# Optimization experiments

Measured on AMD Instinct MI355X. Metric: run time of the kernel, lower is better.

The kernel has to match this reference:

```python
import jax, jax.numpy as jnp
import numpy as np

B, S, DIN, DOUT, A, T, H = 8, 1024, 1024, 1024, 4, 4, 8  # arity A, T cell types, hidden H


def setup_inputs() -> dict:
    key = jax.random.key(0)
    ks = jax.random.split(key, 6)
    x = jax.random.normal(ks[0], (B, S, DIN), jnp.float32)
    sc = 1.0 / np.sqrt(DIN).astype(np.float32)
    weight = jax.random.uniform(ks[1], (A * DOUT, DIN), jnp.float32, -sc, sc)
    bias = jax.random.uniform(ks[2], (A * DOUT,), jnp.float32, -sc, sc)
    # stacked per-cell-type MLP params: arity -> H -> 1 (tanh)
    cw1 = jax.random.normal(ks[3], (T, A, H), jnp.float32) / np.sqrt(A).astype(np.float32)
    cb1 = jnp.zeros((T, H), jnp.float32)
    cw2 = jax.random.normal(ks[4], (T, H), jnp.float32) / np.sqrt(H).astype(np.float32)
    cb2 = jnp.zeros((T,), jnp.float32)
    return {"x": x, "weight": weight, "bias": bias,
            "cw1": cw1, "cb1": cb1, "cw2": cw2, "cb2": cb2}


def reference(x, weight, bias, cw1, cb1, cw2, cb2):
    T_, A_, H_ = cw1.shape
    Dout = weight.shape[0] // A_
    G = Dout // T_  # neurons per cell type (cell_indices = contiguous blocks via np.repeat)
    # all_inputs = F.linear(input, weight, bias): (B, S, A*Dout)
    z = jnp.einsum('bsd,od->bso', x, weight) + bias
    # slice per-neuron arity chunks -> (B, S, T, G, A)
    z = z.reshape(z.shape[0], z.shape[1], T_, G, A_)
    # per-cell-type MLP applied to every neuron of that type (replaces Python loop)
    h = jnp.tanh(jnp.einsum('bstga,tah->bstgh', z, cw1) + cb1[:, None, :])
    o = jnp.einsum('bstgh,th->bstg', h, cw2) + cb2[:, None]
    # concat over neurons -> (B, S, Dout)
    return o.reshape(o.shape[0], o.shape[1], Dout)
```

## Files before the change

kernel.cpp:

```cpp
#include <hip/hip_runtime.h>


typedef __bf16 bf16x8 __attribute__((ext_vector_type(8)));
typedef float f32x4 __attribute__((ext_vector_type(4)));
typedef float f32x16 __attribute__((ext_vector_type(16)));

#define BM 256
#define BN 128
#define BK 32
#define KDIM 1024
#define NT 32
#define ABUF 16384
#define BUFB 24576
#define XN8 (8192 * 1024 / 8)
#define WN8 (4096 * 1024 / 8)

__global__ __launch_bounds__(256) void cvt_bf16_kernel(
    const float* __restrict__ x, const float* __restrict__ w,
    __bf16* __restrict__ xb, __bf16* __restrict__ wb) {
    int i = blockIdx.x * 256 + threadIdx.x;
    const float* src;
    __bf16* dst;
    int j, jdst;
    if (i < XN8) { src = x; dst = xb; j = i; jdst = i; }
    else {
        src = w; dst = wb; j = i - XN8;
        const int r  = j >> 7;
        const int c8 = j & 127;
        const int q  = r >> 2;
        const int a  = r & 3;
        const int rn = ((q >> 5) << 7) + (a << 5) + (q & 31);
        jdst = (rn << 7) + c8;
    }
    const f32x4* p = (const f32x4*)src + 2 * (size_t)j;
    f32x4 a = p[0], b = p[1];
    bf16x8 o;
    o[0] = (__bf16)a[0]; o[1] = (__bf16)a[1]; o[2] = (__bf16)a[2]; o[3] = (__bf16)a[3];
    o[4] = (__bf16)b[0]; o[5] = (__bf16)b[1]; o[6] = (__bf16)b[2]; o[7] = (__bf16)b[3];
    ((bf16x8*)dst)[jdst] = o;
}

__global__ __launch_bounds__(256, 2) void fused_gemm_mlp_kernel(
    const __bf16* __restrict__ Ag,
    const __bf16* __restrict__ Bg,
    const float* __restrict__ bias,
    const float* __restrict__ cw1,
    const float* __restrict__ cb1,
    const float* __restrict__ cw2,
    const float* __restrict__ cb2,
    float* __restrict__ out)
{
    __shared__ __align__(16) unsigned char raw[2 * BUFB];

    const int tid  = threadIdx.x;
    const int wave = tid >> 6;
    const int lane = tid & 63;
    const int wm = wave;
    const int bn0 = blockIdx.x * BN;
    const int bm0 = blockIdx.y * BM;

    f32x16 acc[2][4] = {};

    const int qloc = lane >> 3;
    const int slog = (lane & 7) ^ qloc;
    const int arow = 2 * qloc + (slog >> 2);
    const int acol = (slog & 3) * 8;

    const int lr5 = lane & 31;
    const int lk2 = lane >> 5;
    const int lrh = lr5 >> 1;
    const int lp  = lr5 & 1;
    int a_addr[2], b_addr[2];
#pragma unroll
    for (int kh = 0; kh < 2; ++kh) {
        const int slot = (((lp * 4) + (kh * 2 + lk2)) ^ (lrh & 7)) * 16;
        a_addr[kh] = wm * 4096 + lrh * 128 + slot;
        b_addr[kh] = ABUF + lrh * 128 + slot;
    }
    const char* sb = (const char*)raw;

    auto stage = [&](int t) {
        const int bb = (t & 1) * BUFB;
        const int k0 = t * BK;
#pragma unroll
        for (int c = 0; c < 4; ++c) {
            const int ch = wave + c * 4;
            const __bf16* g = Ag + (size_t)(bm0 + ch * 16 + arow) * KDIM + k0 + acol;
            __builtin_amdgcn_global_load_lds(
                (__attribute__((address_space(1))) void*)g,
                (__attribute__((address_space(3))) void*)&raw[bb + ch * 1024],
                16, 0, 0);
        }
#pragma unroll
        for (int c = 0; c < 2; ++c) {
            const int ch = wave + c * 4;
            const __bf16* g = Bg + (size_t)(bn0 + ch * 16 + arow) * KDIM + k0 + acol;
            __builtin_amdgcn_global_load_lds(
                (__attribute__((address_space(1))) void*)g,
                (__attribute__((address_space(3))) void*)&raw[bb + ABUF + ch * 1024],
                16, 0, 0);
        }
    };

    stage(0);
    __syncthreads();

    for (int t = 0; t < NT; ++t) {
        if (t + 1 < NT) stage(t + 1);

        const int cb = (t & 1) * BUFB;
#pragma unroll
        for (int kh = 0; kh < 2; ++kh) {
            bf16x8 af[2], bfr[4];
#pragma unroll
            for (int mi = 0; mi < 2; ++mi)
                af[mi] = *(const bf16x8*)(sb + cb + a_addr[kh] + mi * 2048);
#pragma unroll
            for (int a = 0; a < 4; ++a)
                bfr[a] = *(const bf16x8*)(sb + cb + b_addr[kh] + a * 2048);
#pragma unroll
            for (int mi = 0; mi < 2; ++mi)
#pragma unroll
                for (int a = 0; a < 4; ++a)
                    acc[mi][a] = __builtin_amdgcn_mfma_f32_32x32x16_bf16(
                        af[mi], bfr[a], acc[mi][a], 0, 0, 0);
        }
        __syncthreads();
    }

    const int tct = bn0 >> 10;
    float w1[32], b1[8], w2[8];
#pragma unroll
    for (int i = 0; i < 32; ++i) w1[i] = cw1[tct * 32 + i];
#pragma unroll
    for (int i = 0; i < 8; ++i) { b1[i] = cb1[tct * 8 + i]; w2[i] = cw2[tct * 8 + i]; }
    const float b2 = cb2[tct];

    const f32x4 bz = *(const f32x4*)&bias[bn0 + 4 * lr5];

    const float L2E2 = 2.885390081777927f;
    float* outp = out + (size_t)(bm0 + wm * 64 + 4 * lk2) * 1024 + (bn0 >> 2) + lr5;

#pragma unroll
    for (int mi = 0; mi < 2; ++mi) {
#pragma unroll
        for (int g = 0; g < 16; ++g) {
            const float z0 = acc[mi][0][g] + bz[0];
            const float z1 = acc[mi][1][g] + bz[1];
            const float z2 = acc[mi][2][g] + bz[2];
            const float z3 = acc[mi][3][g] + bz[3];
            float o = 0.f;
#pragma unroll
            for (int hh = 0; hh < 8; ++hh) {
                float pre = z0 * w1[0 * 8 + hh] + z1 * w1[1 * 8 + hh]
                          + z2 * w1[2 * 8 + hh] + z3 * w1[3 * 8 + hh] + b1[hh];
                float e = __builtin_amdgcn_exp2f(pre * L2E2);
                float th = 1.0f - 2.0f * __builtin_amdgcn_rcpf(e + 1.0f);
                o += th * w2[hh];
            }
            o += b2;
            const int row = mi * 32 + (g & 3) + 8 * (g >> 2);
            outp[(size_t)row * 1024] = o;
        }
    }
}

extern "C" void kernel_launch(void* const* d_in, const int* in_sizes, int n_in,
                              void* d_out, int out_size, void* d_ws, size_t ws_size,
                              hipStream_t stream) {
    const float* x    = (const float*)d_in[0];
    const float* w    = (const float*)d_in[1];
    const float* bias = (const float*)d_in[2];
    const float* cw1  = (const float*)d_in[3];
    const float* cb1  = (const float*)d_in[4];
    const float* cw2  = (const float*)d_in[5];
    const float* cb2  = (const float*)d_in[6];
    float* out = (float*)d_out;

    __bf16* xb = (__bf16*)d_ws;
    __bf16* wb = xb + (size_t)8192 * 1024;

    cvt_bf16_kernel<<<(XN8 + WN8) / 256, 256, 0, stream>>>(x, w, xb, wb);

    dim3 grid(4096 / BN, 8192 / BM);
    fused_gemm_mlp_kernel<<<grid, 256, 0, stream>>>(xb, wb, bias, cw1, cb1, cw2, cb2, out);
}
```

Before: 190.5 us.

## Load weight fragments directly from global in MFMA order, double BK

The convert kernel now writes the bf16 weight in a layout already ordered as MFMA B-fragments, so the GEMM kernel reads B operands straight from global memory (through L1/L2) instead of staging them in LDS. The K tile doubles to 64, halving the iteration count and barrier count, and LDS holds only the A tile. This removes B's LDS traffic and staging work, but each wave now issues global loads on the critical MFMA path, which may expose latency because there is no explicit prefetch.

```diff
diff --git a/kernel.cpp b/kernel.cpp
--- a/kernel.cpp
+++ b/kernel.cpp
@@ -7,11 +7,10 @@
 
 #define BM 256
 #define BN 128
-#define BK 32
+#define BK 64
 #define KDIM 1024
-#define NT 32
-#define ABUF 16384
-#define BUFB 24576
+#define NT 16
+#define ABUF 32768
 #define XN8 (8192 * 1024 / 8)
 #define WN8 (4096 * 1024 / 8)
 
@@ -29,8 +28,12 @@
         const int c8 = j & 127;
         const int q  = r >> 2;
         const int a  = r & 3;
-        const int rn = ((q >> 5) << 7) + (a << 5) + (q & 31);
-        jdst = (rn << 7) + c8;
+        const int nb = q >> 5;
+        const int l5 = q & 31;
+        const int kt = c8 >> 3;
+        const int kh = (c8 >> 1) & 3;
+        const int lk = c8 & 1;
+        jdst = ((((nb * 16 + kt) * 4 + kh) * 4 + a) << 6) + lk * 32 + l5;
     }
     const f32x4* p = (const f32x4*)src + 2 * (size_t)j;
     f32x4 a = p[0], b = p[1];
@@ -50,54 +53,41 @@
     const float* __restrict__ cb2,
     float* __restrict__ out)
 {
-    __shared__ __align__(16) unsigned char raw[2 * BUFB];
+    __shared__ __align__(16) unsigned char raw[2 * ABUF];
 
     const int tid  = threadIdx.x;
     const int wave = tid >> 6;
     const int lane = tid & 63;
-    const int wm = wave;
-    const int bn0 = blockIdx.x * BN;
+    const int nb  = blockIdx.x;
     const int bm0 = blockIdx.y * BM;
+    const int bn0 = nb * BN;
 
     f32x16 acc[2][4] = {};
 
-    const int qloc = lane >> 3;
-    const int slog = (lane & 7) ^ qloc;
-    const int arow = 2 * qloc + (slog >> 2);
-    const int acol = (slog & 3) * 8;
+    const int srow  = lane >> 3;
+    const int scol8 = (((lane & 7) ^ srow) * 8);
 
     const int lr5 = lane & 31;
     const int lk2 = lane >> 5;
-    const int lrh = lr5 >> 1;
-    const int lp  = lr5 & 1;
-    int a_addr[2], b_addr[2];
+    const int lx  = lane & 7;
+    int a_addr[4];
 #pragma unroll
-    for (int kh = 0; kh < 2; ++kh) {
-        const int slot = (((lp * 4) + (kh * 2 + lk2)) ^ (lrh & 7)) * 16;
-        a_addr[kh] = wm * 4096 + lrh * 128 + slot;
-        b_addr[kh] = ABUF + lrh * 128 + slot;
-    }
+    for (int kh = 0; kh < 4; ++kh)
+        a_addr[kh] = (wave * 64 + lr5) * 128 + (((kh * 2 + lk2) ^ lx) * 16);
     const char* sb = (const char*)raw;
 
+    const __bf16* bB = Bg + (size_t)nb * 131072 + lane * 8;
+
     auto stage = [&](int t) {
-        const int bb = (t & 1) * BUFB;
+        const int bb = (t & 1) * ABUF;
         const int k0 = t * BK;
 #pragma unroll
-        for (int c = 0; c < 4; ++c) {
-            const int ch = wave + c * 4;
-            const __bf16* g = Ag + (size_t)(bm0 + ch * 16 + arow) * KDIM + k0 + acol;
+        for (int c = 0; c < 8; ++c) {
+            const int chunk = wave + c * 4;
+            const __bf16* ga = Ag + (size_t)(bm0 + chunk * 8 + srow) * KDIM + k0 + scol8;
             __builtin_amdgcn_global_load_lds(
-                (__attribute__((address_space(1))) void*)g,
-                (__attribute__((address_space(3))) void*)&raw[bb + ch * 1024],
-                16, 0, 0);
-        }
-#pragma unroll
-        for (int c = 0; c < 2; ++c) {
-            const int ch = wave + c * 4;
-            const __bf16* g = Bg + (size_t)(bn0 + ch * 16 + arow) * KDIM + k0 + acol;
-            __builtin_amdgcn_global_load_lds(
-                (__attribute__((address_space(1))) void*)g,
-                (__attribute__((address_space(3))) void*)&raw[bb + ABUF + ch * 1024],
+                (__attribute__((address_space(1))) void*)ga,
+                (__attribute__((address_space(3))) void*)&raw[bb + chunk * 1024],
                 16, 0, 0);
         }
     };
@@ -108,16 +98,17 @@
     for (int t = 0; t < NT; ++t) {
         if (t + 1 < NT) stage(t + 1);
 
-        const int cb = (t & 1) * BUFB;
+        const int cb = (t & 1) * ABUF;
+        const __bf16* bT = bB + t * 8192;
 #pragma unroll
-        for (int kh = 0; kh < 2; ++kh) {
+        for (int kh = 0; kh < 4; ++kh) {
             bf16x8 af[2], bfr[4];
 #pragma unroll
             for (int mi = 0; mi < 2; ++mi)
-                af[mi] = *(const bf16x8*)(sb + cb + a_addr[kh] + mi * 2048);
+                af[mi] = *(const bf16x8*)(sb + cb + a_addr[kh] + mi * 4096);
 #pragma unroll
             for (int a = 0; a < 4; ++a)
-                bfr[a] = *(const bf16x8*)(sb + cb + b_addr[kh] + a * 2048);
+                bfr[a] = *(const bf16x8*)(bT + kh * 2048 + a * 512);
 #pragma unroll
             for (int mi = 0; mi < 2; ++mi)
 #pragma unroll
@@ -125,7 +116,7 @@
                     acc[mi][a] = __builtin_amdgcn_mfma_f32_32x32x16_bf16(
                         af[mi], bfr[a], acc[mi][a], 0, 0, 0);
         }
-        __syncthreads();
+        if (t + 1 < NT) __syncthreads();
     }
 
     const int tct = bn0 >> 10;
@@ -139,7 +130,7 @@
     const f32x4 bz = *(const f32x4*)&bias[bn0 + 4 * lr5];
 
     const float L2E2 = 2.885390081777927f;
-    float* outp = out + (size_t)(bm0 + wm * 64 + 4 * lk2) * 1024 + (bn0 >> 2) + lr5;
+    float* outp = out + (size_t)(bm0 + wave * 64 + 4 * lk2) * 1024 + nb * 32 + lr5;
 
 #pragma unroll
     for (int mi = 0; mi < 2; ++mi) {
```

Result: slower. 197.0 us (+3.4%).
